# Performance work log

Hardware: AMD Instinct MI355X
Metric: run time of the kernel (lower is better)

## Reference

```python
import jax, jax.numpy as jnp
import numpy as np

H = 16       # query heads
KV = 4       # key/value heads
HD = 256     # head dim
ROPE_THETA = 10000.0
EPS = 1e-6


def _rms_norm(x, w):
    # Gemma RMSNorm over last dim: x / rms * (1 + w), computed in fp32
    xf = x.astype(jnp.float32)
    var = jnp.mean(xf * xf, axis=-1, keepdims=True)
    out = xf * jax.lax.rsqrt(var + EPS) * (1.0 + w.astype(jnp.float32))
    return out.astype(x.dtype)


def _rope_cos_sin(position_ids):
    # cos/sin tables of shape [S, HD]
    inv_freq = 1.0 / (ROPE_THETA ** (jnp.arange(0, HD, 2, dtype=jnp.float32) / HD))
    ang = position_ids.astype(jnp.float32)[:, None] * inv_freq[None, :]  # [S, HD/2]
    emb = jnp.concatenate([ang, ang], axis=-1)                           # [S, HD]
    return jnp.cos(emb), jnp.sin(emb)


def _rotate_half(x):
    x1, x2 = jnp.split(x, 2, axis=-1)
    return jnp.concatenate([-x2, x1], axis=-1)


def _apply_rope(x, cos, sin):
    # x: [B, h, S, HD]; cos/sin: [S, HD] -> broadcast over batch and heads
    c = cos[None, None, :, :]
    s = sin[None, None, :, :]
    return (x * c + _rotate_half(x) * s).astype(x.dtype)


def setup_inputs() -> dict:
    key = jax.random.key(0)
    ks = jax.random.split(key, 8)
    B, S, D = 2, 2048, 2048
    inp = {
        "hidden_states": jax.random.normal(ks[0], (B, S, D), jnp.float32),
        "Wq": jax.random.normal(ks[1], (D, H * HD), jnp.float32) * 0.02,
        "Wk": jax.random.normal(ks[2], (D, KV * HD), jnp.float32) * 0.02,
        "Wv": jax.random.normal(ks[3], (D, KV * HD), jnp.float32) * 0.02,
        "Wo": jax.random.normal(ks[4], (H * HD, D), jnp.float32) * 0.02,
        "q_norm_w": jnp.zeros((HD,), jnp.float32),
        "k_norm_w": jnp.zeros((HD,), jnp.float32),
        "position_ids": jnp.arange(S, dtype=jnp.int32),
    }
    return inp


def reference(hidden_states, Wq, Wk, Wv, Wo, q_norm_w, k_norm_w, position_ids):
    B, S, D = hidden_states.shape
    scale = HD ** -0.5

    # projections -> [B, h, S, HD]
    q = jnp.einsum("bsd,de->bse", hidden_states, Wq).reshape(B, S, H, HD).transpose(0, 2, 1, 3)
    k = jnp.einsum("bsd,de->bse", hidden_states, Wk).reshape(B, S, KV, HD).transpose(0, 2, 1, 3)
    v = jnp.einsum("bsd,de->bse", hidden_states, Wv).reshape(B, S, KV, HD).transpose(0, 2, 1, 3)

    # Gemma per-head RMSNorm on q/k
    q = _rms_norm(q, q_norm_w)
    k = _rms_norm(k, k_norm_w)

    # RoPE
    cos, sin = _rope_cos_sin(position_ids)
    q = _apply_rope(q, cos, sin)
    k = _apply_rope(k, cos, sin)

    # GQA: repeat kv heads to match query heads
    rep = H // KV
    k = jnp.repeat(k, rep, axis=1)  # [B, H, S, HD]
    v = jnp.repeat(v, rep, axis=1)

    # SDPA with causal mask, softmax in fp32
    scores = jnp.einsum("bhqd,bhkd->bhqk", q, k) * scale
    causal = jnp.tril(jnp.ones((S, S), dtype=bool))
    scores = jnp.where(causal[None, None, :, :], scores, jnp.finfo(jnp.float32).min)
    probs = jax.nn.softmax(scores.astype(jnp.float32), axis=-1).astype(q.dtype)
    attn = jnp.einsum("bhqk,bhkd->bhqd", probs, v)  # [B, H, S, HD]

    attn = attn.transpose(0, 2, 1, 3).reshape(B, S, H * HD)
    return jnp.einsum("bse,ed->bsd", attn, Wo)
```

## Files before the change

### kernel.cpp

```cpp
#include <hip/hip_runtime.h>

typedef unsigned short ushort_t;
typedef __bf16 bf16_t;
typedef bf16_t bf16x8 __attribute__((ext_vector_type(8)));
typedef float floatx4 __attribute__((ext_vector_type(4)));
typedef ushort_t ushort4v __attribute__((ext_vector_type(4)));
typedef ushort_t ushort8v __attribute__((ext_vector_type(8)));

static constexpr int B = 2, S = 2048, D = 2048;
static constexpr int H = 16, KVH = 4, HD = 256;

#define DEVFN static __device__ __forceinline__

DEVFN ushort_t f2b(float f) {
  union { float f; unsigned u; } x; x.f = f;
  unsigned r = x.u + 0x7fffu + ((x.u >> 16) & 1u);
  return (ushort_t)(r >> 16);
}
DEVFN float b2f(ushort_t h) {
  union { unsigned u; float f; } x; x.u = ((unsigned)h) << 16;
  return x.f;
}
DEVFN void gll16(const void* g, void* l) {
  __builtin_amdgcn_global_load_lds(
      (const __attribute__((address_space(1))) void*)g,
      (__attribute__((address_space(3))) void*)l, 16, 0, 0);
}

DEVFN void bar() {
  asm volatile("" ::: "memory");
  __builtin_amdgcn_s_barrier();
  asm volatile("" ::: "memory");
}
template <int N>
DEVFN void waitvm() { asm volatile("s_waitcnt vmcnt(%0)" ::"n"(N) : "memory"); }

DEVFN ushort4v norm_rope_row(ushort4v raw, const float* __restrict__ w,
                             const float* __restrict__ tab, int s, float scale, int lane) {
  float v[4];
  float ss = 0.f;
#pragma unroll
  for (int i = 0; i < 4; i++) { v[i] = b2f(raw[i]); ss += v[i] * v[i]; }
#pragma unroll
  for (int m = 1; m < 64; m <<= 1) ss += __shfl_xor(ss, m, 64);
  const float inv = rsqrtf(ss * (1.0f / HD) + 1e-6f);
  float4 wv = *(const float4*)(w + lane * 4);
  float y[4];
  y[0] = v[0] * inv * (1.0f + wv.x);
  y[1] = v[1] * inv * (1.0f + wv.y);
  y[2] = v[2] * inv * (1.0f + wv.z);
  y[3] = v[3] * inv * (1.0f + wv.w);
  float py[4];
#pragma unroll
  for (int i = 0; i < 4; i++) py[i] = __shfl_xor(y[i], 32, 64);
  const bool lo = (lane < 32);
  ushort4v ov;
#pragma unroll
  for (int i = 0; i < 4; i++) {
    int dd = (lane * 4 + i) & 127;
    float2 cs = *(const float2*)(tab + ((size_t)s * 128 + dd) * 2);
    float rot = lo ? -py[i] : py[i];
    ov[i] = f2b((y[i] * cs.x + rot * cs.y) * scale);
  }
  return ov;
}

__global__ void k_cvt_bf16(const float* __restrict__ in, ushort_t* __restrict__ out, int n) {
  int i = (blockIdx.x * 256 + threadIdx.x) * 4;
  if (i >= n) return;
  float4 v = *(const float4*)(in + i);
  ushort4v o;
  o[0] = f2b(v.x); o[1] = f2b(v.y); o[2] = f2b(v.z); o[3] = f2b(v.w);
  *(ushort4v*)(out + i) = o;
}

__global__ void k_transpose_cvt(const float* __restrict__ in, ushort_t* __restrict__ out,
                                int R, int C) {
  __shared__ float tile[64][65];
  const int cb = blockIdx.x * 64, rb = blockIdx.y * 64;
  const int t = threadIdx.x;
  const int l16 = t & 15, g16 = t >> 4;
#pragma unroll
  for (int p = 0; p < 4; p++) {
    const int r = p * 16 + g16;
    float4 v = *(const float4*)(in + (size_t)(rb + r) * C + cb + l16 * 4);
    tile[r][l16 * 4 + 0] = v.x;
    tile[r][l16 * 4 + 1] = v.y;
    tile[r][l16 * 4 + 2] = v.z;
    tile[r][l16 * 4 + 3] = v.w;
  }
  __syncthreads();
#pragma unroll
  for (int p = 0; p < 4; p++) {
    const int c = p * 16 + g16;
    ushort4v o4;
#pragma unroll
    for (int i = 0; i < 4; i++) o4[i] = f2b(tile[l16 * 4 + i][c]);
    *(ushort4v*)(out + (size_t)(cb + c) * R + rb + l16 * 4) = o4;
  }
}

__global__ void k_rope_table(const int* __restrict__ pos_ids, float* __restrict__ tab) {
  int idx = blockIdx.x * 256 + threadIdx.x;
  int s = idx >> 7, dd = idx & 127;
  float ang = (float)pos_ids[s] * exp2f((float)dd * (-13.287712379549449f / 128.0f));
  tab[idx * 2] = cosf(ang);
  tab[idx * 2 + 1] = sinf(ang);
}


DEVFN void stage_tile(const ushort_t* __restrict__ A, const ushort_t* __restrict__ Bt,
                      ushort_t* smb, size_t arow0, size_t brow0, int K, int kt) {
  const int t = threadIdx.x;
#pragma unroll
  for (int i = 0; i < 4; i++) {
    const int lin = i * 4096 + t * 8;
    const int ks = i >> 1;
    const int row = ((i & 1) << 7) | (t >> 2);
    const int cs = ((t & 3) * 8) ^ ((row & 8) << 1);
    const size_t gk = (size_t)kt + ks * 32 + cs;
    gll16(A + (arow0 + row) * (size_t)K + gk, smb + lin);
    gll16(Bt + (brow0 + row) * (size_t)K + gk, smb + 16384 + lin);
  }
}

DEVFN bf16x8 lds_frag(const ushort_t* buf, int row, int ks, int lq) {
  const int c = (lq * 8) ^ ((row & 8) << 1);
  return *(const bf16x8*)(buf + ks * 8192 + row * 32 + c);
}

template <int MODE>
__global__ __launch_bounds__(512, 2)
void k_gemm256(const ushort_t* __restrict__ A, const ushort_t* __restrict__ Bt,
               void* __restrict__ C0, void* __restrict__ C1, void* __restrict__ C2,
               int N, int K) {
  __shared__ ushort_t sm[65536];
  const int tid = threadIdx.x;
  const int lane = tid & 63, wave = tid >> 6;
  const int lr = lane & 15, lq = lane >> 4;
  const int wm = wave >> 2, wn = wave & 3;
  const size_t m0 = (size_t)blockIdx.x * 256;
  const size_t n0 = (size_t)blockIdx.y * 256;

  floatx4 acc[8][4];
#pragma unroll
  for (int i = 0; i < 8; i++)
#pragma unroll
    for (int j = 0; j < 4; j++) acc[i][j] = {0.f, 0.f, 0.f, 0.f};

  const int NT = K >> 6;
  stage_tile(A, Bt, sm, m0, n0, K, 0);
  stage_tile(A, Bt, sm + 32768, m0, n0, K, 64);
  waitvm<8>();
  bar();

#pragma unroll 2
  for (int t = 0; t < NT; ++t) {
    const ushort_t* bA = sm + (t & 1) * 32768;
    const ushort_t* bB = bA + 16384;
    bf16x8 a[4][2], bfr[2][2];
#pragma unroll
    for (int r = 0; r < 2; r++)
#pragma unroll
      for (int cq = 0; cq < 2; cq++) {
        if (cq == 0) {
#pragma unroll
          for (int m = 0; m < 4; m++)
#pragma unroll
            for (int ks = 0; ks < 2; ks++)
              a[m][ks] = lds_frag(bA, wm * 128 + r * 64 + m * 16 + lr, ks, lq);
        }
#pragma unroll
        for (int n = 0; n < 2; n++)
#pragma unroll
          for (int ks = 0; ks < 2; ks++)
            bfr[n][ks] = lds_frag(bB, wn * 64 + cq * 32 + n * 16 + lr, ks, lq);
        bar();
        __builtin_amdgcn_s_setprio(1);
#pragma unroll
        for (int ks = 0; ks < 2; ks++)
#pragma unroll
          for (int m = 0; m < 4; m++)
#pragma unroll
            for (int n = 0; n < 2; n++)
              acc[r * 4 + m][cq * 2 + n] = __builtin_amdgcn_mfma_f32_16x16x32_bf16(
                  a[m][ks], bfr[n][ks], acc[r * 4 + m][cq * 2 + n], 0, 0, 0);
        __builtin_amdgcn_s_setprio(0);
        bar();
      }
    if (t + 2 < NT) {
      stage_tile(A, Bt, sm + (t & 1) * 32768, m0, n0, K, (t + 2) * 64);
      waitvm<8>();
    } else {
      waitvm<0>();
    }
    bar();
  }

  const int colb = (int)n0;
#pragma unroll
  for (int mg = 0; mg < 8; mg++)
#pragma unroll
    for (int ng = 0; ng < 4; ng++) {
      const size_t row0 = m0 + wm * 128 + mg * 16 + lq * 4;
      const int col = colb + wn * 64 + ng * 16 + lr;
      if (MODE == 1) {
#pragma unroll
        for (int r = 0; r < 4; r++)
          ((float*)C0)[(row0 + r) * N + col] = acc[mg][ng][r];
      } else {
        if (colb < 4096) {
#pragma unroll
          for (int r = 0; r < 4; r++)
            ((ushort_t*)C0)[(row0 + r) * 4096 + col] = f2b(acc[mg][ng][r]);
        } else if (colb < 5120) {
#pragma unroll
          for (int r = 0; r < 4; r++)
            ((ushort_t*)C1)[(row0 + r) * 1024 + (col - 4096)] = f2b(acc[mg][ng][r]);
        } else {
          const int ch = col - 5120;
          const int kvh = ch >> 8, chh = ch & 255, f = chh >> 4, lrv = chh & 15;
          const size_t bb = row0 >> 11;
          const int s0 = (int)(row0 & 2047);
          const int tile = s0 >> 6, kh = (s0 >> 5) & 1, lqv = (s0 >> 3) & 3, j0 = s0 & 7;
          ushort4v pk;
#pragma unroll
          for (int r = 0; r < 4; r++) pk[r] = f2b(acc[mg][ng][r]);
          *(ushort4v*)&((ushort_t*)C2)[((bb * KVH + kvh) * (S / 64) + tile) * 16384 +
                                       (size_t)(f * 2 + kh) * 512 +
                                       (size_t)(lqv * 16 + lrv) * 8 + j0] = pk;
        }
      }
    }
}

__global__ void k_norm_rope(ushort_t* __restrict__ x, const float* __restrict__ w,
                            const float* __restrict__ tab, int heads, float scale) {
  const int lane = threadIdx.x & 63;
  const size_t row = (size_t)blockIdx.x * 4 + (threadIdx.x >> 6);
  const int s = (int)((row / heads) % S);
  ushort_t* p = x + row * HD + lane * 4;
  ushort4v raw = *(const ushort4v*)p;
  *(ushort4v*)p = norm_rope_row(raw, w, tab, s, scale, lane);
}

__global__ void k_norm_rope_k(const ushort_t* __restrict__ Kb, ushort_t* __restrict__ Kf,
                              const float* __restrict__ w, const float* __restrict__ tab) {
  __shared__ ushort_t t[64 * 264];
  const int lane = threadIdx.x & 63, wave = threadIdx.x >> 6;
  const int tile = blockIdx.x, kvh = blockIdx.y, b = blockIdx.z;
#pragma unroll
  for (int rr = 0; rr < 16; rr++) {
    const int row = wave * 16 + rr;
    const int s = tile * 64 + row;
    const ushort_t* p = Kb + ((size_t)(b * S + s) * KVH + kvh) * HD + lane * 4;
    ushort4v raw = *(const ushort4v*)p;
    *(ushort4v*)&t[row * 264 + lane * 4] = norm_rope_row(raw, w, tab, s, 1.0f, lane);
  }
  __syncthreads();
  ushort_t* dst = Kf + ((size_t)(b * KVH + kvh) * (S / 64) + tile) * 16384;
  const int lr = lane & 15, lq = lane >> 4;
#pragma unroll
  for (int q = 0; q < 8; q++) {
    const int c = wave * 8 + q;
    const int nt = c >> 3, ks = c & 7;
    ushort8v v = *(const ushort8v*)&t[(nt * 16 + lr) * 264 + ks * 32 + lq * 8];
    *(ushort8v*)&dst[(size_t)c * 512 + lane * 8] = v;
  }
}

__global__ __launch_bounds__(256, 2)
void k_attn(const ushort_t* __restrict__ Q, const ushort_t* __restrict__ Kf,
            const ushort_t* __restrict__ Vf, ushort_t* __restrict__ O) {
  __shared__ ushort_t Ks[32 * 512];
  __shared__ ushort_t Vs[32 * 512];
  __shared__ ushort_t Ps[4][16 * 72];
  const int lane = threadIdx.x & 63, wave = threadIdx.x >> 6;
  const int lr = lane & 15, lq = lane >> 4;
  const int h = blockIdx.y, b = blockIdx.z;
  const int kvh = h >> 2;
  const size_t kvb = (size_t)(b * KVH + kvh) * (S / 64);

#pragma unroll 1
  for (int half = 0; half < 2; half++) {
    const int qt = half ? (int)blockIdx.x : (S / 64 - 1 - (int)blockIdx.x);
    const int q0 = qt * 64 + wave * 16;

    bf16x8 qf[8];
    {
      const ushort_t* qp = Q + ((size_t)(b * S + q0 + lr) * H + h) * HD + lq * 8;
#pragma unroll
      for (int ks = 0; ks < 8; ks++) qf[ks] = *(const bf16x8*)(qp + ks * 32);
    }
    floatx4 o[16];
#pragma unroll
    for (int f = 0; f < 16; f++) o[f] = {0.f, 0.f, 0.f, 0.f};
    float m_i[4] = {-1e30f, -1e30f, -1e30f, -1e30f};
    float l_i[4] = {0.f, 0.f, 0.f, 0.f};

    const int ntiles = qt + 1;
    for (int kt = 0; kt < ntiles; kt++) {
      const int kbase = kt * 64;
      __syncthreads();
      const ushort_t* tb = Kf + (kvb + kt) * 16384;
      const ushort_t* vb = Vf + (kvb + kt) * 16384;
#pragma unroll
      for (int i = 0; i < 16; i++) {
        const int c = wave * 16 + i;
        if (c < 32) gll16(tb + (size_t)c * 512 + lane * 8, &Ks[c * 512 + lane * 8]);
        else        gll16(vb + (size_t)(c - 32) * 512 + lane * 8, &Vs[(c - 32) * 512 + lane * 8]);
      }
      __syncthreads();

      const int ntmax = min(4, ((q0 + 15 - kbase) >> 4) + 1);
      floatx4 sacc[4];
#pragma unroll
      for (int nt = 0; nt < 4; nt++) {
        if (nt < ntmax) {
          sacc[nt] = {0.f, 0.f, 0.f, 0.f};
#pragma unroll
          for (int ks = 0; ks < 8; ks++) {
            bf16x8 kf = *(const bf16x8*)&Ks[(nt * 8 + ks) * 512 + lane * 8];
            sacc[nt] = __builtin_amdgcn_mfma_f32_16x16x32_bf16(qf[ks], kf, sacc[nt], 0, 0, 0);
          }
        } else {
          sacc[nt] = {-1e30f, -1e30f, -1e30f, -1e30f};
        }
      }
      if (kbase + 63 > q0) {
#pragma unroll
        for (int nt = 0; nt < 4; nt++)
          if (nt < ntmax)
#pragma unroll
            for (int r = 0; r < 4; r++)
              if (kbase + nt * 16 + lr > q0 + lq * 4 + r) sacc[nt][r] = -1e30f;
      }
      float mt[4], alpha[4], rs[4];
#pragma unroll
      for (int r = 0; r < 4; r++)
        mt[r] = fmaxf(fmaxf(sacc[0][r], sacc[1][r]), fmaxf(sacc[2][r], sacc[3][r]));
#pragma unroll
      for (int m = 1; m < 16; m <<= 1)
#pragma unroll
        for (int r = 0; r < 4; r++) mt[r] = fmaxf(mt[r], __shfl_xor(mt[r], m, 64));
#pragma unroll
      for (int r = 0; r < 4; r++) {
        float mn = fmaxf(m_i[r], mt[r]);
        alpha[r] = exp2f(m_i[r] - mn);
        m_i[r] = mn;
      }
#pragma unroll
      for (int nt = 0; nt < 4; nt++)
#pragma unroll
        for (int r = 0; r < 4; r++) sacc[nt][r] = exp2f(sacc[nt][r] - m_i[r]);
#pragma unroll
      for (int r = 0; r < 4; r++)
        rs[r] = (sacc[0][r] + sacc[1][r]) + (sacc[2][r] + sacc[3][r]);
#pragma unroll
      for (int m = 1; m < 16; m <<= 1)
#pragma unroll
        for (int r = 0; r < 4; r++) rs[r] += __shfl_xor(rs[r], m, 64);
#pragma unroll
      for (int r = 0; r < 4; r++) l_i[r] = l_i[r] * alpha[r] + rs[r];
      if (__any((alpha[0] < 1.f) | (alpha[1] < 1.f) | (alpha[2] < 1.f) | (alpha[3] < 1.f))) {
#pragma unroll
        for (int f = 0; f < 16; f++) {
          o[f][0] *= alpha[0]; o[f][1] *= alpha[1];
          o[f][2] *= alpha[2]; o[f][3] *= alpha[3];
        }
      }
      ushort_t* psw = Ps[wave];
#pragma unroll
      for (int nt = 0; nt < 4; nt++)
#pragma unroll
        for (int r = 0; r < 4; r++)
          psw[(lq * 4 + r) * 72 + nt * 16 + lr] = f2b(sacc[nt][r]);
      bf16x8 pf0 = *(const bf16x8*)&psw[lr * 72 + lq * 8];
      bf16x8 pf1 = *(const bf16x8*)&psw[lr * 72 + 32 + lq * 8];
#pragma unroll
      for (int f = 0; f < 16; f++) {
        bf16x8 vf0 = *(const bf16x8*)&Vs[(f * 2 + 0) * 512 + lane * 8];
        o[f] = __builtin_amdgcn_mfma_f32_16x16x32_bf16(pf0, vf0, o[f], 0, 0, 0);
        bf16x8 vf1 = *(const bf16x8*)&Vs[(f * 2 + 1) * 512 + lane * 8];
        o[f] = __builtin_amdgcn_mfma_f32_16x16x32_bf16(pf1, vf1, o[f], 0, 0, 0);
      }
    }
    float invl[4];
#pragma unroll
    for (int r = 0; r < 4; r++) invl[r] = 1.0f / l_i[r];
#pragma unroll
    for (int f = 0; f < 16; f++)
#pragma unroll
      for (int r = 0; r < 4; r++)
        O[((size_t)(b * S + q0 + lq * 4 + r) * H + h) * HD + f * 16 + lr] =
            f2b(o[f][r] * invl[r]);
  }
}

extern "C" void kernel_launch(void* const* d_in, const int* in_sizes, int n_in,
                              void* d_out, int out_size, void* d_ws, size_t ws_size,
                              hipStream_t stream) {
  const float* hs = (const float*)d_in[0];
  const float* Wq = (const float*)d_in[1];
  const float* Wk = (const float*)d_in[2];
  const float* Wv = (const float*)d_in[3];
  const float* Wo = (const float*)d_in[4];
  const float* qw = (const float*)d_in[5];
  const float* kw = (const float*)d_in[6];
  const int* pos = (const int*)d_in[7];
  float* out = (float*)d_out;

  char* ws = (char*)d_ws;
  size_t off = 0;
  auto alloc = [&](size_t bytes) {
    void* p = ws + off;
    off += (bytes + 255) & ~(size_t)255;
    return p;
  };
  ushort_t* Xb   = (ushort_t*)alloc((size_t)B * S * D * 2);
  ushort_t* Wqt  = (ushort_t*)alloc((size_t)(H * HD) * D * 2);
  ushort_t* Wkvt = (ushort_t*)alloc((size_t)(2 * KVH * HD) * D * 2);
  ushort_t* Wot  = (ushort_t*)alloc((size_t)D * (H * HD) * 2);
  ushort_t* Qb   = (ushort_t*)alloc((size_t)B * S * H * HD * 2);
  ushort_t* Kf   = (ushort_t*)alloc((size_t)B * S * KVH * HD * 2);
  ushort_t* Vf   = (ushort_t*)alloc((size_t)B * S * KVH * HD * 2);
  ushort_t* Ab   = (ushort_t*)alloc((size_t)B * S * H * HD * 2);
  float*    tab  = (float*)alloc((size_t)S * 128 * 2 * sizeof(float));
  ushort_t* Kb = Ab;

  k_cvt_bf16<<<(B * S * D / 4 + 255) / 256, 256, 0, stream>>>(hs, Xb, B * S * D);
  k_transpose_cvt<<<dim3((H * HD) / 64, D / 64), 256, 0, stream>>>(Wq, Wqt, D, H * HD);
  k_transpose_cvt<<<dim3((KVH * HD) / 64, D / 64), 256, 0, stream>>>(Wk, Wkvt, D, KVH * HD);
  k_transpose_cvt<<<dim3((KVH * HD) / 64, D / 64), 256, 0, stream>>>(
      Wv, Wkvt + (size_t)(KVH * HD) * D, D, KVH * HD);
  k_transpose_cvt<<<dim3(D / 64, (H * HD) / 64), 256, 0, stream>>>(Wo, Wot, H * HD, D);
  k_rope_table<<<S * 128 / 256, 256, 0, stream>>>(pos, tab);

  k_gemm256<0><<<dim3((B * S) / 256, 6144 / 256), 512, 0, stream>>>(
      Xb, Wqt, Qb, Kb, Vf, 6144, D);

  k_norm_rope<<<B * S * H / 4, 256, 0, stream>>>(Qb, qw, tab, H, 0.0625f * 1.4426950408889634f);
  k_norm_rope_k<<<dim3(S / 64, KVH, B), 256, 0, stream>>>(Kb, Kf, kw, tab);

  k_attn<<<dim3(S / 128, H, B), 256, 0, stream>>>(Qb, Kf, Vf, Ab);

  k_gemm256<1><<<dim3((B * S) / 256, D / 256), 512, 0, stream>>>(
      Ab, Wot, out, nullptr, nullptr, D, H * HD);
}
```

Measured before the change: 623.8 us.

## Shrink GEMM tile to 128x256 and overlap next-tile staging with MFMAs

```diff
diff --git a/kernel.cpp b/kernel.cpp
--- a/kernel.cpp
+++ b/kernel.cpp
@@ -112,21 +112,29 @@
 DEVFN void stage_tile(const ushort_t* __restrict__ A, const ushort_t* __restrict__ Bt,
                       ushort_t* smb, size_t arow0, size_t brow0, int K, int kt) {
   const int t = threadIdx.x;
+  const int rq = t >> 2;
+  const int cq = (t & 3) * 8;
+#pragma unroll
+  for (int i = 0; i < 2; i++) {
+    const int cs = cq ^ ((rq & 8) << 1);
+    gll16(A + (arow0 + rq) * (size_t)K + kt + i * 32 + cs, smb + i * 4096 + t * 8);
+  }
 #pragma unroll
   for (int i = 0; i < 4; i++) {
-    const int lin = i * 4096 + t * 8;
-    const int ks = i >> 1;
-    const int row = ((i & 1) << 7) | (t >> 2);
-    const int cs = ((t & 3) * 8) ^ ((row & 8) << 1);
-    const size_t gk = (size_t)kt + ks * 32 + cs;
-    gll16(A + (arow0 + row) * (size_t)K + gk, smb + lin);
-    gll16(Bt + (brow0 + row) * (size_t)K + gk, smb + 16384 + lin);
-  }
-}
-
-DEVFN bf16x8 lds_frag(const ushort_t* buf, int row, int ks, int lq) {
+    const int row = ((i & 1) << 7) | rq;
+    const int cs = cq ^ ((row & 8) << 1);
+    gll16(Bt + (brow0 + row) * (size_t)K + kt + (i >> 1) * 32 + cs,
+          smb + 8192 + i * 4096 + t * 8);
+  }
+}
+
+DEVFN bf16x8 ldsA(const ushort_t* buf, int row, int ks, int lq) {
   const int c = (lq * 8) ^ ((row & 8) << 1);
-  return *(const bf16x8*)(buf + ks * 8192 + row * 32 + c);
+  return *(const bf16x8*)(buf + ks * 4096 + row * 32 + c);
+}
+DEVFN bf16x8 ldsB(const ushort_t* buf, int row, int ks, int lq) {
+  const int c = (lq * 8) ^ ((row & 8) << 1);
+  return *(const bf16x8*)(buf + 8192 + ks * 8192 + row * 32 + c);
 }
 
 template <int MODE>
@@ -134,75 +142,64 @@
 void k_gemm256(const ushort_t* __restrict__ A, const ushort_t* __restrict__ Bt,
                void* __restrict__ C0, void* __restrict__ C1, void* __restrict__ C2,
                int N, int K) {
-  __shared__ ushort_t sm[65536];
+  __shared__ ushort_t sm[49152];
   const int tid = threadIdx.x;
   const int lane = tid & 63, wave = tid >> 6;
   const int lr = lane & 15, lq = lane >> 4;
   const int wm = wave >> 2, wn = wave & 3;
-  const size_t m0 = (size_t)blockIdx.x * 256;
+  const size_t m0 = (size_t)blockIdx.x * 128;
   const size_t n0 = (size_t)blockIdx.y * 256;
 
-  floatx4 acc[8][4];
-#pragma unroll
-  for (int i = 0; i < 8; i++)
+  floatx4 acc[4][4];
+#pragma unroll
+  for (int i = 0; i < 4; i++)
 #pragma unroll
     for (int j = 0; j < 4; j++) acc[i][j] = {0.f, 0.f, 0.f, 0.f};
 
   const int NT = K >> 6;
   stage_tile(A, Bt, sm, m0, n0, K, 0);
-  stage_tile(A, Bt, sm + 32768, m0, n0, K, 64);
-  waitvm<8>();
-  bar();
-
-#pragma unroll 2
+  stage_tile(A, Bt, sm + 24576, m0, n0, K, 64);
+
   for (int t = 0; t < NT; ++t) {
-    const ushort_t* bA = sm + (t & 1) * 32768;
-    const ushort_t* bB = bA + 16384;
-    bf16x8 a[4][2], bfr[2][2];
-#pragma unroll
-    for (int r = 0; r < 2; r++)
-#pragma unroll
-      for (int cq = 0; cq < 2; cq++) {
-        if (cq == 0) {
-#pragma unroll
-          for (int m = 0; m < 4; m++)
-#pragma unroll
-            for (int ks = 0; ks < 2; ks++)
-              a[m][ks] = lds_frag(bA, wm * 128 + r * 64 + m * 16 + lr, ks, lq);
-        }
-#pragma unroll
-        for (int n = 0; n < 2; n++)
-#pragma unroll
-          for (int ks = 0; ks < 2; ks++)
-            bfr[n][ks] = lds_frag(bB, wn * 64 + cq * 32 + n * 16 + lr, ks, lq);
-        bar();
-        __builtin_amdgcn_s_setprio(1);
-#pragma unroll
-        for (int ks = 0; ks < 2; ks++)
-#pragma unroll
-          for (int m = 0; m < 4; m++)
-#pragma unroll
-            for (int n = 0; n < 2; n++)
-              acc[r * 4 + m][cq * 2 + n] = __builtin_amdgcn_mfma_f32_16x16x32_bf16(
-                  a[m][ks], bfr[n][ks], acc[r * 4 + m][cq * 2 + n], 0, 0, 0);
-        __builtin_amdgcn_s_setprio(0);
-        bar();
-      }
-    if (t + 2 < NT) {
-      stage_tile(A, Bt, sm + (t & 1) * 32768, m0, n0, K, (t + 2) * 64);
-      waitvm<8>();
-    } else {
-      waitvm<0>();
+    ushort_t* bA = sm + (t & 1) * 24576;
+    if (t < NT - 1) waitvm<6>(); else waitvm<0>();
+    bar();
+
+    bf16x8 a[2][4], bfr[2][4];
+#pragma unroll
+    for (int ks = 0; ks < 2; ks++) {
+#pragma unroll
+      for (int m = 0; m < 4; m++) a[ks][m] = ldsA(bA, wm * 64 + m * 16 + lr, ks, lq);
+#pragma unroll
+      for (int n = 0; n < 4; n++) bfr[ks][n] = ldsB(bA, wn * 64 + n * 16 + lr, ks, lq);
     }
+    __builtin_amdgcn_s_setprio(1);
+#pragma unroll
+    for (int m = 0; m < 4; m++)
+#pragma unroll
+      for (int n = 0; n < 4; n++)
+        acc[m][n] = __builtin_amdgcn_mfma_f32_16x16x32_bf16(a[0][m], bfr[0][n], acc[m][n], 0, 0, 0);
+    __builtin_amdgcn_s_setprio(0);
+    asm volatile("s_waitcnt lgkmcnt(0)" ::: "memory");
+    __builtin_amdgcn_sched_barrier(0);
     bar();
+    if (t + 2 < NT) stage_tile(A, Bt, bA, m0, n0, K, (t + 2) * 64);
+    __builtin_amdgcn_sched_barrier(0);
+    __builtin_amdgcn_s_setprio(1);
+#pragma unroll
+    for (int m = 0; m < 4; m++)
+#pragma unroll
+      for (int n = 0; n < 4; n++)
+        acc[m][n] = __builtin_amdgcn_mfma_f32_16x16x32_bf16(a[1][m], bfr[1][n], acc[m][n], 0, 0, 0);
+    __builtin_amdgcn_s_setprio(0);
   }
 
   const int colb = (int)n0;
 #pragma unroll
-  for (int mg = 0; mg < 8; mg++)
+  for (int mg = 0; mg < 4; mg++)
 #pragma unroll
     for (int ng = 0; ng < 4; ng++) {
-      const size_t row0 = m0 + wm * 128 + mg * 16 + lq * 4;
+      const size_t row0 = m0 + wm * 64 + mg * 16 + lq * 4;
       const int col = colb + wn * 64 + ng * 16 + lr;
       if (MODE == 1) {
 #pragma unroll
@@ -436,7 +433,7 @@
   k_transpose_cvt<<<dim3(D / 64, (H * HD) / 64), 256, 0, stream>>>(Wo, Wot, H * HD, D);
   k_rope_table<<<S * 128 / 256, 256, 0, stream>>>(pos, tab);
 
-  k_gemm256<0><<<dim3((B * S) / 256, 6144 / 256), 512, 0, stream>>>(
+  k_gemm256<0><<<dim3((B * S) / 128, 6144 / 256), 512, 0, stream>>>(
       Xb, Wqt, Qb, Kb, Vf, 6144, D);
 
   k_norm_rope<<<B * S * H / 4, 256, 0, stream>>>(Qb, qw, tab, H, 0.0625f * 1.4426950408889634f);
@@ -444,6 +441,6 @@
 
   k_attn<<<dim3(S / 128, H, B), 256, 0, stream>>>(Qb, Kf, Vf, Ab);
 
-  k_gemm256<1><<<dim3((B * S) / 256, D / 256), 512, 0, stream>>>(
+  k_gemm256<1><<<dim3((B * S) / 128, D / 256), 512, 0, stream>>>(
       Ab, Wot, out, nullptr, nullptr, D, H * HD);
 }
```

Measured after the change: 509.8 us. 18.3% less time.
